# Performance work log

Hardware: AMD Instinct MI355X
Metric: run time of the kernel (lower is better)

## Reference

```python
import jax, jax.numpy as jnp
import numpy as np

N_NODES = 100000
D_NODE = 80
N_EDGES = 1600000


def setup_inputs() -> dict:
    key = jax.random.key(0)
    ks = jax.random.split(key, 8)
    nodeEmbed = jax.random.normal(ks[0], (N_NODES, D_NODE), dtype=jnp.float32)
    edge_index = jax.random.randint(ks[1], (2, N_EDGES), 0, N_NODES, dtype=jnp.int32)
    # Linear params (fan-in scaled)
    W1 = jax.random.normal(ks[2], (161, 32), dtype=jnp.float32) / np.sqrt(161.0)
    b1 = jax.random.normal(ks[3], (32,), dtype=jnp.float32) * 0.01
    W2 = jax.random.normal(ks[4], (32, 32), dtype=jnp.float32) / np.sqrt(32.0)
    b2 = jax.random.normal(ks[5], (32,), dtype=jnp.float32) * 0.01
    W3 = jax.random.normal(ks[6], (32, 2), dtype=jnp.float32) / np.sqrt(32.0)
    b3 = jax.random.normal(ks[7], (2,), dtype=jnp.float32) * 0.01
    return {"nodeEmbed": nodeEmbed, "edge_index": edge_index,
            "W1": W1, "b1": b1, "W2": W2, "b2": b2, "W3": W3, "b3": b3}


def reference(nodeEmbed, edge_index, W1, b1, W2, b2, W3, b3):
    # embedEdges: gather src/dst node embeddings, concat with constant edge feat
    x_src = nodeEmbed[edge_index[0]]          # [E, 80]
    x_dst = nodeEmbed[edge_index[1]]          # [E, 80]
    edge_feats = jnp.ones((edge_index.shape[1], 1), dtype=nodeEmbed.dtype)
    edge_embed = jnp.concatenate([x_src, edge_feats, x_dst], axis=-1)  # [E, 161]
    # forward: lin1 -> relu -> lin2 -> relu -> lin3 -> log_softmax
    h = jax.nn.relu(edge_embed @ W1 + b1)     # [E, 32]
    h = jax.nn.relu(h @ W2 + b2)              # [E, 32]
    logits = h @ W3 + b3                      # [E, 2]
    return jax.nn.log_softmax(logits, axis=1)
```

## Files before the change

kernel.cpp:

```cpp
#include <hip/hip_runtime.h>
#include <hip/hip_bf16.h>

#define D_NODE 80
#define EDGE_ITERS 4

typedef __attribute__((ext_vector_type(8))) short short8;
typedef __attribute__((ext_vector_type(16))) float f32x16;

__device__ __forceinline__ float bf16lo(unsigned u) {
    return __uint_as_float(u << 16);
}
__device__ __forceinline__ float bf16hi(unsigned u) {
    return __uint_as_float(u & 0xffff0000u);
}
__device__ __forceinline__ unsigned packbf2(float a, float b) {
    __hip_bfloat162 h = __float22bfloat162_rn(make_float2(a, b));
    union { __hip_bfloat162 h2; unsigned u; } cv; cv.h2 = h;
    return cv.u;
}
__device__ __forceinline__ short f2bf(float f) {
    __hip_bfloat16 h = __float2bfloat16(f);
    union { __hip_bfloat16 h1; short s; } cv; cv.h1 = h;
    return cv.s;
}

__global__ __launch_bounds__(256) void proj_kernel(
    const float* __restrict__ X, const float* __restrict__ W1,
    const float* __restrict__ b1,
    unsigned short* __restrict__ PS, unsigned short* __restrict__ PD, int N)
{
    const int lane = threadIdx.x & 63;
    const int wave = threadIdx.x >> 6;
    const int n    = lane & 31;
    const int hi   = lane >> 5;

    short8 Ws[5], Wd[5];
#pragma unroll
    for (int s = 0; s < 5; ++s) {
#pragma unroll
        for (int j = 0; j < 8; ++j) {
            int k = s * 16 + hi * 8 + j;
            Ws[s][j] = f2bf(W1[k * 32 + n]);
            Wd[s][j] = f2bf(W1[(81 + k) * 32 + n]);
        }
    }
    float cdInit[16];
#pragma unroll
    for (int r = 0; r < 16; ++r) {
        int f = (r & 3) + 8 * (r >> 2) + 4 * hi;
        cdInit[r] = b1[f] + W1[80 * 32 + f];
    }

    const int tiles = N / 32;
    for (int tile = blockIdx.x * 4 + wave; tile < tiles; tile += gridDim.x * 4) {
        const int node = tile * 32 + n;
        const float4* xrow = (const float4*)(X + (size_t)node * D_NODE + hi * 8);

        f32x16 cs, cd;
#pragma unroll
        for (int r = 0; r < 16; ++r) { cs[r] = 0.0f; cd[r] = cdInit[r]; }

#pragma unroll
        for (int s = 0; s < 5; ++s) {
            float4 xa = xrow[s * 4];
            float4 xb = xrow[s * 4 + 1];
            union { uint4 u; short8 s8; } Bx;
            Bx.u.x = packbf2(xa.x, xa.y);
            Bx.u.y = packbf2(xa.z, xa.w);
            Bx.u.z = packbf2(xb.x, xb.y);
            Bx.u.w = packbf2(xb.z, xb.w);
            cs = __builtin_amdgcn_mfma_f32_32x32x16_bf16(Ws[s], Bx.s8, cs, 0, 0, 0);
            cd = __builtin_amdgcn_mfma_f32_32x32x16_bf16(Wd[s], Bx.s8, cd, 0, 0, 0);
        }

        unsigned short* psr = PS + (size_t)node * 32 + hi * 4;
        unsigned short* pdr = PD + (size_t)node * 32 + hi * 4;
#pragma unroll
        for (int q = 0; q < 4; ++q) {
            uint2 vs = make_uint2(packbf2(cs[4*q+0], cs[4*q+1]),
                                  packbf2(cs[4*q+2], cs[4*q+3]));
            uint2 vd = make_uint2(packbf2(cd[4*q+0], cd[4*q+1]),
                                  packbf2(cd[4*q+2], cd[4*q+3]));
            *(uint2*)(psr + q * 8) = vs;
            *(uint2*)(pdr + q * 8) = vd;
        }
    }
}

__global__ __launch_bounds__(256) void edge_kernel(
    const int* __restrict__ ei,
    const unsigned short* __restrict__ PS, const unsigned short* __restrict__ PD,
    const float* __restrict__ W2, const float* __restrict__ b2,
    const float* __restrict__ W3, const float* __restrict__ b3,
    float* __restrict__ out, int E)
{
    const int tid  = threadIdx.x;
    const int wave = tid >> 6;
    const int lane = tid & 63;
    const int n    = lane & 31;
    const int hi   = lane >> 5;

    short8 Wa0, Wa1;
#pragma unroll
    for (int j = 0; j < 8; ++j) {
        int k0 = hi * 8 + j;
        Wa0[j] = f2bf(W2[k0 * 32 + n]);
        Wa1[j] = f2bf(W2[(16 + k0) * 32 + n]);
    }
    unsigned b2p[8], w3p[16];
#pragma unroll
    for (int r = 0; r < 16; ++r) {
        int row = (r & 3) + 8 * (r >> 2) + 4 * hi;
        w3p[r] = packbf2(W3[row * 2 + 0], W3[row * 2 + 1]);
        if ((r & 1) == 0) {
            int row2 = ((r + 1) & 3) + 8 * ((r + 1) >> 2) + 4 * hi;
            b2p[r >> 1] = packbf2(b2[row], b2[row2]);
        }
    }
    const float b30 = b3[0], b31 = b3[1];

    const long base = ((long)blockIdx.x * 4 + wave) * (32 * EDGE_ITERS);

    int sIdx[EDGE_ITERS], dIdx[EDGE_ITERS];
#pragma unroll
    for (int it = 0; it < EDGE_ITERS; ++it) {
        long e = base + (long)it * 32 + n;
        int ec = (e < E) ? (int)e : 0;
        sIdx[it] = ei[ec];
        dIdx[it] = ei[(size_t)E + ec];
    }

    uint4 av0[EDGE_ITERS], av1[EDGE_ITERS], bv0[EDGE_ITERS], bv1[EDGE_ITERS];
#pragma unroll
    for (int it = 0; it < EDGE_ITERS; ++it) {
        av0[it] = *(const uint4*)(PS + (size_t)sIdx[it] * 32 + hi * 8);
        av1[it] = *(const uint4*)(PS + (size_t)sIdx[it] * 32 + 16 + hi * 8);
        bv0[it] = *(const uint4*)(PD + (size_t)dIdx[it] * 32 + hi * 8);
        bv1[it] = *(const uint4*)(PD + (size_t)dIdx[it] * 32 + 16 + hi * 8);
    }

#pragma unroll
    for (int it = 0; it < EDGE_ITERS; ++it) {
        union { uint4 u; short8 s8; } B0, B1;
        B0.u.x = packbf2(fmaxf(bf16lo(av0[it].x) + bf16lo(bv0[it].x), 0.f),
                         fmaxf(bf16hi(av0[it].x) + bf16hi(bv0[it].x), 0.f));
        B0.u.y = packbf2(fmaxf(bf16lo(av0[it].y) + bf16lo(bv0[it].y), 0.f),
                         fmaxf(bf16hi(av0[it].y) + bf16hi(bv0[it].y), 0.f));
        B0.u.z = packbf2(fmaxf(bf16lo(av0[it].z) + bf16lo(bv0[it].z), 0.f),
                         fmaxf(bf16hi(av0[it].z) + bf16hi(bv0[it].z), 0.f));
        B0.u.w = packbf2(fmaxf(bf16lo(av0[it].w) + bf16lo(bv0[it].w), 0.f),
                         fmaxf(bf16hi(av0[it].w) + bf16hi(bv0[it].w), 0.f));
        B1.u.x = packbf2(fmaxf(bf16lo(av1[it].x) + bf16lo(bv1[it].x), 0.f),
                         fmaxf(bf16hi(av1[it].x) + bf16hi(bv1[it].x), 0.f));
        B1.u.y = packbf2(fmaxf(bf16lo(av1[it].y) + bf16lo(bv1[it].y), 0.f),
                         fmaxf(bf16hi(av1[it].y) + bf16hi(bv1[it].y), 0.f));
        B1.u.z = packbf2(fmaxf(bf16lo(av1[it].z) + bf16lo(bv1[it].z), 0.f),
                         fmaxf(bf16hi(av1[it].z) + bf16hi(bv1[it].z), 0.f));
        B1.u.w = packbf2(fmaxf(bf16lo(av1[it].w) + bf16lo(bv1[it].w), 0.f),
                         fmaxf(bf16hi(av1[it].w) + bf16hi(bv1[it].w), 0.f));

        f32x16 c;
#pragma unroll
        for (int q = 0; q < 8; ++q) {
            c[2*q]   = bf16lo(b2p[q]);
            c[2*q+1] = bf16hi(b2p[q]);
        }
        c = __builtin_amdgcn_mfma_f32_32x32x16_bf16(Wa0, B0.s8, c, 0, 0, 0);
        c = __builtin_amdgcn_mfma_f32_32x32x16_bf16(Wa1, B1.s8, c, 0, 0, 0);

        float p0 = 0.f, p1 = 0.f;
#pragma unroll
        for (int r = 0; r < 16; ++r) {
            float h = fmaxf(c[r], 0.f);
            p0 += h * bf16lo(w3p[r]);
            p1 += h * bf16hi(w3p[r]);
        }
        p0 += __shfl_xor(p0, 32, 64);
        p1 += __shfl_xor(p1, 32, 64);

        if (hi == 0) {
            long eo = base + (long)it * 32 + n;
            if (eo < E) {
                float l0 = p0 + b30;
                float l1 = p1 + b31;
                float mm = fmaxf(l0, l1);
                float z  = __expf(l0 - mm) + __expf(l1 - mm);
                float lse = mm + __logf(z);
                *(float2*)(out + 2 * eo) = make_float2(l0 - lse, l1 - lse);
            }
        }
    }
}

extern "C" void kernel_launch(void* const* d_in, const int* in_sizes, int n_in,
                              void* d_out, int out_size, void* d_ws, size_t ws_size,
                              hipStream_t stream) {
    const float* X  = (const float*)d_in[0];
    const int*   ei = (const int*)d_in[1];
    const float* W1 = (const float*)d_in[2];
    const float* b1 = (const float*)d_in[3];
    const float* W2 = (const float*)d_in[4];
    const float* b2 = (const float*)d_in[5];
    const float* W3 = (const float*)d_in[6];
    const float* b3 = (const float*)d_in[7];
    float* out = (float*)d_out;

    int N = in_sizes[0] / D_NODE;
    int E = in_sizes[1] / 2;

    unsigned short* PS = (unsigned short*)d_ws;
    unsigned short* PD = PS + (size_t)N * 32;

    int ptiles = (N / 32 + 3) / 4;
    proj_kernel<<<ptiles, 256, 0, stream>>>(X, W1, b1, PS, PD, N);

    int edges_per_block = 4 * 32 * EDGE_ITERS;
    int nblk = (E + edges_per_block - 1) / edges_per_block;
    edge_kernel<<<nblk, 256, 0, stream>>>(ei, PS, PD, W2, b2, W3, b3, out, E);
}
```

Before: 66.66 us.

## Prefetch next node tile in projection kernel with persistent grid; halve edge iters

The projection kernel now runs as a fixed 256-block persistent grid. Each wave loads the first tile's node rows before loading weights, then prefetches the next tile's rows into registers while computing the current one, which hides global load latency behind the MFMA work. Edges handled per wave in the edge kernel are halved, giving more, smaller blocks. The trade-offs are higher register pressure from the prefetch buffers and possibly lower parallelism in the projection stage with only 256 blocks.

```diff
diff --git a/kernel.cpp b/kernel.cpp
--- a/kernel.cpp
+++ b/kernel.cpp
@@ -2,7 +2,7 @@
 #include <hip/hip_bf16.h>
 
 #define D_NODE 80
-#define EDGE_ITERS 4
+#define EDGE_ITERS 2
 
 typedef __attribute__((ext_vector_type(8))) short short8;
 typedef __attribute__((ext_vector_type(16))) float f32x16;
@@ -34,6 +34,18 @@
     const int n    = lane & 31;
     const int hi   = lane >> 5;
 
+    const int tiles  = N / 32;
+    const int stride = gridDim.x * 4;
+    int tile = blockIdx.x * 4 + wave;
+    if (tile >= tiles) return;
+
+    float4 xc[10];
+    {
+        const float4* xrow = (const float4*)(X + (size_t)(tile * 32 + n) * D_NODE + hi * 8);
+#pragma unroll
+        for (int s = 0; s < 5; ++s) { xc[2*s] = xrow[s*4]; xc[2*s+1] = xrow[s*4+1]; }
+    }
+
     short8 Ws[5], Wd[5];
 #pragma unroll
     for (int s = 0; s < 5; ++s) {
@@ -51,10 +63,14 @@
         cdInit[r] = b1[f] + W1[80 * 32 + f];
     }
 
-    const int tiles = N / 32;
-    for (int tile = blockIdx.x * 4 + wave; tile < tiles; tile += gridDim.x * 4) {
-        const int node = tile * 32 + n;
-        const float4* xrow = (const float4*)(X + (size_t)node * D_NODE + hi * 8);
+    while (tile < tiles) {
+        const int nt = tile + stride;
+        float4 xn[10];
+        if (nt < tiles) {
+            const float4* xrow = (const float4*)(X + (size_t)(nt * 32 + n) * D_NODE + hi * 8);
+#pragma unroll
+            for (int s = 0; s < 5; ++s) { xn[2*s] = xrow[s*4]; xn[2*s+1] = xrow[s*4+1]; }
+        }
 
         f32x16 cs, cd;
 #pragma unroll
@@ -62,17 +78,16 @@
 
 #pragma unroll
         for (int s = 0; s < 5; ++s) {
-            float4 xa = xrow[s * 4];
-            float4 xb = xrow[s * 4 + 1];
             union { uint4 u; short8 s8; } Bx;
-            Bx.u.x = packbf2(xa.x, xa.y);
-            Bx.u.y = packbf2(xa.z, xa.w);
-            Bx.u.z = packbf2(xb.x, xb.y);
-            Bx.u.w = packbf2(xb.z, xb.w);
+            Bx.u.x = packbf2(xc[2*s].x, xc[2*s].y);
+            Bx.u.y = packbf2(xc[2*s].z, xc[2*s].w);
+            Bx.u.z = packbf2(xc[2*s+1].x, xc[2*s+1].y);
+            Bx.u.w = packbf2(xc[2*s+1].z, xc[2*s+1].w);
             cs = __builtin_amdgcn_mfma_f32_32x32x16_bf16(Ws[s], Bx.s8, cs, 0, 0, 0);
             cd = __builtin_amdgcn_mfma_f32_32x32x16_bf16(Wd[s], Bx.s8, cd, 0, 0, 0);
         }
 
+        const int node = tile * 32 + n;
         unsigned short* psr = PS + (size_t)node * 32 + hi * 4;
         unsigned short* pdr = PD + (size_t)node * 32 + hi * 4;
 #pragma unroll
@@ -84,6 +99,10 @@
             *(uint2*)(psr + q * 8) = vs;
             *(uint2*)(pdr + q * 8) = vd;
         }
+
+#pragma unroll
+        for (int i = 0; i < 10; ++i) xc[i] = xn[i];
+        tile = nt;
     }
 }
 
@@ -211,8 +230,7 @@
     unsigned short* PS = (unsigned short*)d_ws;
     unsigned short* PD = PS + (size_t)N * 32;
 
-    int ptiles = (N / 32 + 3) / 4;
-    proj_kernel<<<ptiles, 256, 0, stream>>>(X, W1, b1, PS, PD, N);
+    proj_kernel<<<256, 256, 0, stream>>>(X, W1, b1, PS, PD, N);
 
     int edges_per_block = 4 * 32 * EDGE_ITERS;
     int nblk = (E + edges_per_block - 1) / edges_per_block;
```

Result: faster. 61.23 us (-8.2%).
